# Optimization experiments

Measured on AMD Instinct MI355X. Metric: run time of the kernel, lower is better.

## Reference

```python
import jax, jax.numpy as jnp
import numpy as np

N_HEADS = 16
HEAD_DIM = 64  # dim=1024 / n_heads=16


def setup_inputs() -> dict:
    key = jax.random.key(0)
    ks = jax.random.split(key, 7)
    B, S, D = 4, 2048, 1024
    scale = 1.0 / np.sqrt(D)
    return {
        "q": jax.random.normal(ks[0], (B, S, D), jnp.float32),
        "k": jax.random.normal(ks[1], (B, S, D), jnp.float32),
        "v": jax.random.normal(ks[2], (B, S, D), jnp.float32),
        "Wq": jax.random.normal(ks[3], (D, D), jnp.float32) * scale,
        "Wk": jax.random.normal(ks[4], (D, D), jnp.float32) * scale,
        "Wv": jax.random.normal(ks[5], (D, D), jnp.float32) * scale,
        "Wo": jax.random.normal(ks[6], (D, D), jnp.float32) * scale,
    }


def reference(q, k, v, Wq, Wk, Wv, Wo):
    B, S, _ = q.shape
    H, Dh = N_HEADS, HEAD_DIM
    # linear projections (torch Linear: x @ W.T), reshape to [B, H, S, Dh]
    xq = (q @ Wq.T).reshape(B, S, H, Dh).transpose(0, 2, 1, 3)
    xk = (k @ Wk.T).reshape(B, S, H, Dh).transpose(0, 2, 1, 3)
    xv = (v @ Wv.T).reshape(B, S, H, Dh).transpose(0, 2, 1, 3)
    scores = jnp.einsum("bhsd,bhtd->bhst", xq, xk) / jnp.sqrt(jnp.float32(Dh))
    # causal mask: -inf above diagonal
    causal = jnp.triu(jnp.full((S, S), -jnp.inf, jnp.float32), k=1)
    scores = scores + causal[None, None]
    attn = jax.nn.softmax(scores.astype(jnp.float32), axis=-1).astype(xq.dtype)
    out = jnp.einsum("bhst,bhtd->bhsd", attn, xv)
    out = out.transpose(0, 2, 1, 3).reshape(B, S, H * Dh)
    return out @ Wo.T
```

## Files before the change

kernel.cpp:

```cpp
#include <hip/hip_runtime.h>
#include <hip/hip_bf16.h>

#define DI __device__ __forceinline__

typedef __attribute__((ext_vector_type(8))) short short8;
typedef __attribute__((ext_vector_type(4))) short short4v;
typedef __attribute__((ext_vector_type(4))) float f32x4;

#define QSCALE 0.180336885f

DI short f2bf(float f) {
  unsigned u = __builtin_bit_cast(unsigned, f);
  unsigned r = u + 0x7fffu + ((u >> 16) & 1u);
  return (short)(r >> 16);
}

DI float fexp2(float x) {
#if __has_builtin(__builtin_amdgcn_exp2f)
  return __builtin_amdgcn_exp2f(x);
#else
  return exp2f(x);
#endif
}

DI void gl16(const short* g, short* l) {
  __builtin_amdgcn_global_load_lds(
      (const __attribute__((address_space(1))) void*)g,
      (__attribute__((address_space(3))) void*)l, 16, 0, 0);
}

__global__ __launch_bounds__(256) void convert_w(
    const float* __restrict__ wq, const float* __restrict__ wk,
    const float* __restrict__ wv, const float* __restrict__ wo,
    short* __restrict__ dst) {
  int z = blockIdx.z;
  const float* src = (z == 0) ? wq : (z == 1) ? wk : (z == 2) ? wv : wo;
  short* d = dst + (size_t)z * 1024 * 1024;
  int i = (blockIdx.x * 256 + threadIdx.x) * 4;
  float4 f = *(const float4*)(src + i);
  short4v v;
  v[0] = f2bf(f.x); v[1] = f2bf(f.y); v[2] = f2bf(f.z); v[3] = f2bf(f.w);
  *(short4v*)(d + i) = v;
}

__global__ __launch_bounds__(256) void convert_x(
    const float* __restrict__ q, const float* __restrict__ k,
    const float* __restrict__ v, short* __restrict__ qb,
    short* __restrict__ kb, short* __restrict__ vb) {
  int z = blockIdx.z;
  const float* src = (z == 0) ? q : (z == 1) ? k : v;
  short* dst = (z == 0) ? qb : (z == 1) ? kb : vb;
  size_t i = ((size_t)blockIdx.x * 256 + threadIdx.x) * 8;
  float4 f0 = *(const float4*)(src + i);
  float4 f1 = *(const float4*)(src + i + 4);
  short8 o;
  o[0] = f2bf(f0.x); o[1] = f2bf(f0.y); o[2] = f2bf(f0.z); o[3] = f2bf(f0.w);
  o[4] = f2bf(f1.x); o[5] = f2bf(f1.y); o[6] = f2bf(f1.z); o[7] = f2bf(f1.w);
  *(short8*)(dst + i) = o;
}

__global__ __launch_bounds__(256) void convert_one(
    const float* __restrict__ src, short* __restrict__ dst) {
  size_t i = ((size_t)blockIdx.x * 256 + threadIdx.x) * 8;
  float4 f0 = *(const float4*)(src + i);
  float4 f1 = *(const float4*)(src + i + 4);
  short8 o;
  o[0] = f2bf(f0.x); o[1] = f2bf(f0.y); o[2] = f2bf(f0.z); o[3] = f2bf(f0.w);
  o[4] = f2bf(f1.x); o[5] = f2bf(f1.y); o[6] = f2bf(f1.z); o[7] = f2bf(f1.w);
  *(short8*)(dst + i) = o;
}

enum { OUT_F32 = 0, OUT_HEAD = 1, OUT_HEADT = 2 };

template <int OMODE>
DI void gemm_core(const short* __restrict__ A, const short* __restrict__ B,
                  void* __restrict__ Cp, float scale, int bm, int bn) {
  __shared__ __align__(16) short sA[128 * 64];
  __shared__ __align__(16) short sB[128 * 64];

  const int tid = threadIdx.x;
  const int lane = tid & 63;
  const int wid = tid >> 6;
  const int wm = wid >> 1, wn = wid & 1;
  const int l15 = lane & 15, lq = lane >> 4;
  const int lrr = lane >> 3;
  const int lch = lane & 7;

  f32x4 acc[4][4] = {};

  for (int k0 = 0; k0 < 1024; k0 += 64) {
#pragma unroll
    for (int i = 0; i < 4; ++i) {
      int r0 = wid * 32 + i * 8;
      int rr = r0 + lrr;
      int sc = (lch ^ (rr & 7)) << 3;
      gl16(A + (size_t)(bm + rr) * 1024 + k0 + sc, sA + r0 * 64);
      gl16(B + (size_t)(bn + rr) * 1024 + k0 + sc, sB + r0 * 64);
    }
    __syncthreads();

#pragma unroll
    for (int ks = 0; ks < 2; ++ks) {
      short8 a[4], b[4];
#pragma unroll
      for (int mt = 0; mt < 4; ++mt) {
        int row = wm * 64 + mt * 16 + l15;
        int off = (row * 128 + ks * 64 + lq * 16) ^ ((row & 7) << 4);
        a[mt] = *(const short8*)((const char*)sA + off);
      }
#pragma unroll
      for (int nt = 0; nt < 4; ++nt) {
        int row = wn * 64 + nt * 16 + l15;
        int off = (row * 128 + ks * 64 + lq * 16) ^ ((row & 7) << 4);
        b[nt] = *(const short8*)((const char*)sB + off);
      }
#pragma unroll
      for (int mt = 0; mt < 4; ++mt)
#pragma unroll
        for (int nt = 0; nt < 4; ++nt) {
          if (OMODE == OUT_HEADT)
            acc[mt][nt] = __builtin_amdgcn_mfma_f32_16x16x32_bf16(
                b[nt], a[mt], acc[mt][nt], 0, 0, 0);
          else
            acc[mt][nt] = __builtin_amdgcn_mfma_f32_16x16x32_bf16(
                a[mt], b[nt], acc[mt][nt], 0, 0, 0);
        }
    }
    __syncthreads();
  }

#pragma unroll
  for (int mt = 0; mt < 4; ++mt) {
#pragma unroll
    for (int nt = 0; nt < 4; ++nt) {
#pragma unroll
      for (int r = 0; r < 4; ++r) {
        float val = acc[mt][nt][r] * scale;
        if (OMODE == OUT_HEADT) {
          int f = bn + wn * 64 + nt * 16 + lq * 4 + r;
          int t = bm + wm * 64 + mt * 16 + l15;
          int bb = t >> 11, s = t & 2047;
          int h = f >> 6, dh = f & 63;
          ((short*)Cp)[((size_t)((bb * 16 + h) * 64 + dh)) * 2048 + s] = f2bf(val);
        } else {
          int rowg = bm + wm * 64 + mt * 16 + lq * 4 + r;
          int colg = bn + wn * 64 + nt * 16 + l15;
          if (OMODE == OUT_HEAD) {
            int bb = rowg >> 11, s = rowg & 2047;
            int h = colg >> 6, dh = colg & 63;
            ((short*)Cp)[((size_t)(bb * 16 + h) * 2048 + s) * 64 + dh] = f2bf(val);
          } else {
            ((float*)Cp)[(size_t)rowg * 1024 + colg] = val;
          }
        }
      }
    }
  }
}

DI void xcd_map(int id, int& bm, int& bn) {
  int xcd = id & 7, slot = id >> 3;
  int panel = xcd + 8 * (slot >> 3);
  int ntile = slot & 7;
  bm = panel * 128;
  bn = ntile * 128;
}

__global__ __launch_bounds__(256) void proj_gemm3(
    const short* __restrict__ qb, const short* __restrict__ kb,
    const short* __restrict__ vb, const short* __restrict__ wq,
    const short* __restrict__ wk, const short* __restrict__ wv,
    short* __restrict__ xq, short* __restrict__ xk, short* __restrict__ xvT) {
  int z = blockIdx.z;
  int bm, bn;
  xcd_map(blockIdx.x, bm, bn);
  if (z == 0) {
    gemm_core<OUT_HEAD>(qb, wq, xq, QSCALE, bm, bn);
  } else if (z == 1) {
    gemm_core<OUT_HEAD>(kb, wk, xk, 1.0f, bm, bn);
  } else {
    gemm_core<OUT_HEADT>(vb, wv, xvT, 1.0f, bm, bn);
  }
}

__global__ __launch_bounds__(256) void proj_oneN(
    const short* __restrict__ A, const short* __restrict__ B,
    short* __restrict__ C, float scale) {
  int bm, bn;
  xcd_map(blockIdx.x, bm, bn);
  gemm_core<OUT_HEAD>(A, B, C, scale, bm, bn);
}

__global__ __launch_bounds__(256) void proj_oneT(
    const short* __restrict__ A, const short* __restrict__ B,
    short* __restrict__ C, float scale) {
  int bm, bn;
  xcd_map(blockIdx.x, bm, bn);
  gemm_core<OUT_HEADT>(A, B, C, scale, bm, bn);
}

__global__ __launch_bounds__(256) void final_gemm(
    const short* __restrict__ oa, const short* __restrict__ wo,
    float* __restrict__ out) {
  int bm, bn;
  xcd_map(blockIdx.x, bm, bn);
  gemm_core<OUT_F32>(oa, wo, out, 1.0f, bm, bn);
}

__global__ __launch_bounds__(256, 4) void attn_k(
    const short* __restrict__ Xq, const short* __restrict__ Xk,
    const short* __restrict__ XvT, short* __restrict__ Oa) {
  __shared__ __align__(16) short sK[2][64 * 64];
  __shared__ __align__(16) short sVT[2][64 * 64];
  __shared__ __align__(16) short sP[4][16 * 64];

  const int tid = threadIdx.x;
  const int lane = tid & 63;
  const int wid = tid >> 6;
  const int l15 = lane & 15, lq = lane >> 4;
  const int bid = blockIdx.x;
  const int ipair = bid >> 6;
  const int bh = bid & 63;
  const int b = bh >> 4, h = bh & 15;

  const short* Q = Xq + (size_t)bh * 2048 * 64;
  const short* K = Xk + (size_t)bh * 2048 * 64;
  const short* VT = XvT + (size_t)bh * 64 * 2048;

  const int srow = tid >> 3;
  const int scol = (tid & 7) * 8;
  const int soff0 = (srow * 128 + scol * 2) ^ ((srow & 7) << 4);
  const int soff1 = ((srow + 32) * 128 + scol * 2) ^ ((srow & 7) << 4);

  short8 kreg[2], vreg[2];
  kreg[0] = *(const short8*)(K + (size_t)srow * 64 + scol);
  kreg[1] = *(const short8*)(K + (size_t)(srow + 32) * 64 + scol);
  vreg[0] = *(const short8*)(VT + (size_t)srow * 2048 + scol);
  vreg[1] = *(const short8*)(VT + (size_t)(srow + 32) * 2048 + scol);

  *(short8*)((char*)sK[0] + soff0) = kreg[0];
  *(short8*)((char*)sK[0] + soff1) = kreg[1];
  *(short8*)((char*)sVT[0] + soff0) = vreg[0];
  *(short8*)((char*)sVT[0] + soff1) = vreg[1];

  short* sPw = sP[wid];
  int p = 0;

  for (int seg = 0; seg < 2; ++seg) {
    const int qt = seg ? ipair : (31 - ipair);
    const int qrow0 = qt * 64 + wid * 16;
    const int qg = qrow0 + l15;

    short8 qf[2];
#pragma unroll
    for (int ks = 0; ks < 2; ++ks)
      qf[ks] = *(const short8*)(Q + (size_t)qg * 64 + ks * 32 + lq * 8);

    float m_run = -1e30f, l_run = 0.f;
    f32x4 acc[4] = {};

    for (int kt = 0; kt <= qt; ++kt) {
      const int kv0 = kt * 64;
      __syncthreads();

      int nkt = kt + 1, nseg = seg;
      if (nkt > qt) { nseg = seg + 1; nkt = 0; }
      const bool hn = (nseg < 2);
      if (hn) {
        const int kn = nkt * 64;
        kreg[0] = *(const short8*)(K + (size_t)(kn + srow) * 64 + scol);
        kreg[1] = *(const short8*)(K + (size_t)(kn + srow + 32) * 64 + scol);
        vreg[0] = *(const short8*)(VT + (size_t)srow * 2048 + kn + scol);
        vreg[1] = *(const short8*)(VT + (size_t)(srow + 32) * 2048 + kn + scol);
      }

      const char* bufK = (const char*)sK[p];
      const char* bufV = (const char*)sVT[p];

      f32x4 sc[4] = {};
      __builtin_amdgcn_s_setprio(1);
#pragma unroll
      for (int ks = 0; ks < 2; ++ks) {
        short8 kf[4];
#pragma unroll
        for (int nt = 0; nt < 4; ++nt) {
          int row = nt * 16 + l15;
          int off = (row * 128 + ks * 64 + lq * 16) ^ ((row & 7) << 4);
          kf[nt] = *(const short8*)(bufK + off);
        }
#pragma unroll
        for (int nt = 0; nt < 4; ++nt)
          sc[nt] = __builtin_amdgcn_mfma_f32_16x16x32_bf16(kf[nt], qf[ks], sc[nt], 0, 0, 0);
      }
      __builtin_amdgcn_s_setprio(0);

      float pv[4][4];
      float m = -1e30f;
      const bool diag = (kt == qt);
#pragma unroll
      for (int nt = 0; nt < 4; ++nt) {
#pragma unroll
        for (int r = 0; r < 4; ++r) {
          float s = sc[nt][r];
          if (diag && (kv0 + nt * 16 + lq * 4 + r > qg)) s = -1e30f;
          pv[nt][r] = s;
          m = fmaxf(m, s);
        }
      }
      m = fmaxf(m, __shfl_xor(m, 16));
      m = fmaxf(m, __shfl_xor(m, 32));

      if (!__all(m - m_run <= 8.0f)) {
        const float m_new = fmaxf(m_run, m);
        const float corr = fexp2(m_run - m_new);
        l_run *= corr;
#pragma unroll
        for (int mt = 0; mt < 4; ++mt)
#pragma unroll
          for (int r = 0; r < 4; ++r) acc[mt][r] *= corr;
        m_run = m_new;
      }

      float rsum = 0.f;
#pragma unroll
      for (int nt = 0; nt < 4; ++nt)
#pragma unroll
        for (int r = 0; r < 4; ++r) {
          float e = fexp2(pv[nt][r] - m_run);
          pv[nt][r] = e;
          rsum += e;
        }
      rsum += __shfl_xor(rsum, 16);
      rsum += __shfl_xor(rsum, 32);
      l_run += rsum;

#pragma unroll
      for (int nt = 0; nt < 4; ++nt) {
        short4v pw;
#pragma unroll
        for (int r = 0; r < 4; ++r) pw[r] = f2bf(pv[nt][r]);
        int off = (l15 * 128 + nt * 32 + lq * 8) ^ ((l15 & 7) << 4);
        *(short4v*)((char*)sPw + off) = pw;
      }

      __builtin_amdgcn_s_setprio(1);
#pragma unroll
      for (int ks = 0; ks < 2; ++ks) {
        int poff = (l15 * 128 + ks * 64 + lq * 16) ^ ((l15 & 7) << 4);
        short8 pf = *(const short8*)((const char*)sPw + poff);
#pragma unroll
        for (int mt = 0; mt < 4; ++mt) {
          int row = mt * 16 + l15;
          int voff = (row * 128 + ks * 64 + lq * 16) ^ ((row & 7) << 4);
          short8 vf = *(const short8*)(bufV + voff);
          acc[mt] = __builtin_amdgcn_mfma_f32_16x16x32_bf16(vf, pf, acc[mt], 0, 0, 0);
        }
      }
      __builtin_amdgcn_s_setprio(0);

      if (hn) {
        *(short8*)((char*)sK[p ^ 1] + soff0) = kreg[0];
        *(short8*)((char*)sK[p ^ 1] + soff1) = kreg[1];
        *(short8*)((char*)sVT[p ^ 1] + soff0) = vreg[0];
        *(short8*)((char*)sVT[p ^ 1] + soff1) = vreg[1];
      }
      p ^= 1;
    }

    const float rl = 1.0f / l_run;
    short* orow = Oa + ((size_t)(b * 2048 + qg)) * 1024 + h * 64;
#pragma unroll
    for (int mt = 0; mt < 4; ++mt) {
      short4v o;
#pragma unroll
      for (int r = 0; r < 4; ++r) o[r] = f2bf(acc[mt][r] * rl);
      *(short4v*)(orow + mt * 16 + lq * 4) = o;
    }
  }
}

extern "C" void kernel_launch(void* const* d_in, const int* in_sizes, int n_in,
                              void* d_out, int out_size, void* d_ws,
                              size_t ws_size, hipStream_t stream) {
  const float* q = (const float*)d_in[0];
  const float* k = (const float*)d_in[1];
  const float* v = (const float*)d_in[2];
  const float* Wq = (const float*)d_in[3];
  const float* Wk = (const float*)d_in[4];
  const float* Wv = (const float*)d_in[5];
  const float* Wo = (const float*)d_in[6];

  char* ws = (char*)d_ws;
  short* wq_b = (short*)(ws + (0ull << 20));
  short* wk_b = (short*)(ws + (2ull << 20));
  short* wv_b = (short*)(ws + (4ull << 20));
  short* wo_b = (short*)(ws + (6ull << 20));
  short* xq  = (short*)(ws + (8ull << 20));
  short* xk  = (short*)(ws + (24ull << 20));
  short* xvT = (short*)(ws + (56ull << 20));

  convert_w<<<dim3(1024, 1, 4), 256, 0, stream>>>(Wq, Wk, Wv, Wo, wq_b);

  if (ws_size >= (122ull << 20)) {
    short* qb = (short*)(ws + (72ull << 20));
    short* kb = (short*)(ws + (88ull << 20));
    short* vb = (short*)(ws + (104ull << 20));
    short* oa = qb;

    convert_x<<<dim3(4096, 1, 3), 256, 0, stream>>>(q, k, v, qb, kb, vb);
    proj_gemm3<<<dim3(512, 1, 3), 256, 0, stream>>>(qb, kb, vb, wq_b, wk_b,
                                                    wv_b, xq, xk, xvT);
    attn_k<<<dim3(1024), 256, 0, stream>>>(xq, xk, xvT, oa);
    final_gemm<<<dim3(512), 256, 0, stream>>>(oa, wo_b, (float*)d_out);
  } else {
    short* X = (short*)(ws + (8ull << 20));
    short* xq2 = (short*)(ws + (24ull << 20));
    short* xk2 = (short*)(ws + (40ull << 20));
    short* xvT2 = (short*)(ws + (56ull << 20));
    short* oa2 = (short*)(ws + (72ull << 20));

    convert_one<<<dim3(4096), 256, 0, stream>>>(q, X);
    proj_oneN<<<dim3(512), 256, 0, stream>>>(X, wq_b, xq2, QSCALE);
    convert_one<<<dim3(4096), 256, 0, stream>>>(k, X);
    proj_oneN<<<dim3(512), 256, 0, stream>>>(X, wk_b, xk2, 1.0f);
    convert_one<<<dim3(4096), 256, 0, stream>>>(v, X);
    proj_oneT<<<dim3(512), 256, 0, stream>>>(X, wv_b, xvT2, 1.0f);
    attn_k<<<dim3(1024), 256, 0, stream>>>(xq2, xk2, xvT2, oa2);
    final_gemm<<<dim3(512), 256, 0, stream>>>(oa2, wo_b, (float*)d_out);
  }
}
```

Before: 184.6 us.

## Use 128-row query tiles with 512-thread attention blocks sharing K/V tiles

The attention kernel now processes 128 query rows per block with 8 waves (512 threads) instead of 64 rows with 4 waves. Each staged K/V tile is therefore reused by twice as many queries, and the grid is halved. Waves whose rows lie entirely above a KV tile skip its compute, and masking is applied only on tiles that cross the diagonal. The bf16 conversion helper is switched to the library intrinsic. In exchange there are fewer blocks, load imbalance inside a block along the diagonal, and register pressure under launch bounds of 512 threads with 4 blocks per CU.

```diff
diff --git a/kernel.cpp b/kernel.cpp
--- a/kernel.cpp
+++ b/kernel.cpp
@@ -10,9 +10,8 @@
 #define QSCALE 0.180336885f
 
 DI short f2bf(float f) {
-  unsigned u = __builtin_bit_cast(unsigned, f);
-  unsigned r = u + 0x7fffu + ((u >> 16) & 1u);
-  return (short)(r >> 16);
+  __hip_bfloat16 h = __float2bfloat16(f);
+  return __builtin_bit_cast(short, h);
 }
 
 DI float fexp2(float x) {
@@ -207,12 +206,12 @@
   gemm_core<OUT_F32>(oa, wo, out, 1.0f, bm, bn);
 }
 
-__global__ __launch_bounds__(256, 4) void attn_k(
+__global__ __launch_bounds__(512, 4) void attn_k(
     const short* __restrict__ Xq, const short* __restrict__ Xk,
     const short* __restrict__ XvT, short* __restrict__ Oa) {
   __shared__ __align__(16) short sK[2][64 * 64];
   __shared__ __align__(16) short sVT[2][64 * 64];
-  __shared__ __align__(16) short sP[4][16 * 64];
+  __shared__ __align__(16) short sP[8][16 * 64];
 
   const int tid = threadIdx.x;
   const int lane = tid & 63;
@@ -229,27 +228,24 @@
 
   const int srow = tid >> 3;
   const int scol = (tid & 7) * 8;
-  const int soff0 = (srow * 128 + scol * 2) ^ ((srow & 7) << 4);
-  const int soff1 = ((srow + 32) * 128 + scol * 2) ^ ((srow & 7) << 4);
-
-  short8 kreg[2], vreg[2];
-  kreg[0] = *(const short8*)(K + (size_t)srow * 64 + scol);
-  kreg[1] = *(const short8*)(K + (size_t)(srow + 32) * 64 + scol);
-  vreg[0] = *(const short8*)(VT + (size_t)srow * 2048 + scol);
-  vreg[1] = *(const short8*)(VT + (size_t)(srow + 32) * 2048 + scol);
-
-  *(short8*)((char*)sK[0] + soff0) = kreg[0];
-  *(short8*)((char*)sK[0] + soff1) = kreg[1];
-  *(short8*)((char*)sVT[0] + soff0) = vreg[0];
-  *(short8*)((char*)sVT[0] + soff1) = vreg[1];
+  const int soff = (srow * 128 + scol * 2) ^ ((srow & 7) << 4);
+
+  short8 kreg, vreg;
+  kreg = *(const short8*)(K + (size_t)srow * 64 + scol);
+  vreg = *(const short8*)(VT + (size_t)srow * 2048 + scol);
+
+  *(short8*)((char*)sK[0] + soff) = kreg;
+  *(short8*)((char*)sVT[0] + soff) = vreg;
 
   short* sPw = sP[wid];
   int p = 0;
 
   for (int seg = 0; seg < 2; ++seg) {
-    const int qt = seg ? ipair : (31 - ipair);
-    const int qrow0 = qt * 64 + wid * 16;
-    const int qg = qrow0 + l15;
+    const int qt = seg ? ipair : (15 - ipair);
+    const int qfirst = qt * 128 + wid * 16;
+    const int qg = qfirst + l15;
+    const int qlast = qfirst + 15;
+    const int ntile = 2 * qt + 2;
 
     short8 qf[2];
 #pragma unroll
@@ -259,110 +255,121 @@
     float m_run = -1e30f, l_run = 0.f;
     f32x4 acc[4] = {};
 
-    for (int kt = 0; kt <= qt; ++kt) {
+    for (int kt = 0; kt < ntile; ++kt) {
       const int kv0 = kt * 64;
       __syncthreads();
 
       int nkt = kt + 1, nseg = seg;
-      if (nkt > qt) { nseg = seg + 1; nkt = 0; }
+      if (nkt >= ntile) { nseg = seg + 1; nkt = 0; }
       const bool hn = (nseg < 2);
       if (hn) {
         const int kn = nkt * 64;
-        kreg[0] = *(const short8*)(K + (size_t)(kn + srow) * 64 + scol);
-        kreg[1] = *(const short8*)(K + (size_t)(kn + srow + 32) * 64 + scol);
-        vreg[0] = *(const short8*)(VT + (size_t)srow * 2048 + kn + scol);
-        vreg[1] = *(const short8*)(VT + (size_t)(srow + 32) * 2048 + kn + scol);
-      }
-
-      const char* bufK = (const char*)sK[p];
-      const char* bufV = (const char*)sVT[p];
-
-      f32x4 sc[4] = {};
-      __builtin_amdgcn_s_setprio(1);
-#pragma unroll
-      for (int ks = 0; ks < 2; ++ks) {
-        short8 kf[4];
+        kreg = *(const short8*)(K + (size_t)(kn + srow) * 64 + scol);
+        vreg = *(const short8*)(VT + (size_t)srow * 2048 + kn + scol);
+      }
+
+      const bool fullmask = (kv0 > qlast);
+      if (!fullmask) {
+        const bool needmask = (kv0 + 63 > qfirst);
+        const char* bufK = (const char*)sK[p];
+        const char* bufV = (const char*)sVT[p];
+
+        f32x4 sc[4] = {};
+        __builtin_amdgcn_s_setprio(1);
+#pragma unroll
+        for (int ks = 0; ks < 2; ++ks) {
+          short8 kf[4];
+#pragma unroll
+          for (int nt = 0; nt < 4; ++nt) {
+            int row = nt * 16 + l15;
+            int off = (row * 128 + ks * 64 + lq * 16) ^ ((row & 7) << 4);
+            kf[nt] = *(const short8*)(bufK + off);
+          }
+#pragma unroll
+          for (int nt = 0; nt < 4; ++nt)
+            sc[nt] = __builtin_amdgcn_mfma_f32_16x16x32_bf16(kf[nt], qf[ks],
+                                                             sc[nt], 0, 0, 0);
+        }
+        __builtin_amdgcn_s_setprio(0);
+
+        float pv[4][4];
+        float m = -1e30f;
+        if (needmask) {
+#pragma unroll
+          for (int nt = 0; nt < 4; ++nt)
+#pragma unroll
+            for (int r = 0; r < 4; ++r) {
+              float s = sc[nt][r];
+              if (kv0 + nt * 16 + lq * 4 + r > qg) s = -1e30f;
+              pv[nt][r] = s;
+              m = fmaxf(m, s);
+            }
+        } else {
+#pragma unroll
+          for (int nt = 0; nt < 4; ++nt)
+#pragma unroll
+            for (int r = 0; r < 4; ++r) {
+              float s = sc[nt][r];
+              pv[nt][r] = s;
+              m = fmaxf(m, s);
+            }
+        }
+        m = fmaxf(m, __shfl_xor(m, 16));
+        m = fmaxf(m, __shfl_xor(m, 32));
+
+        if (!__all(m - m_run <= 8.0f)) {
+          const float m_new = fmaxf(m_run, m);
+          const float corr = fexp2(m_run - m_new);
+          l_run *= corr;
+#pragma unroll
+          for (int mt = 0; mt < 4; ++mt)
+#pragma unroll
+            for (int r = 0; r < 4; ++r) acc[mt][r] *= corr;
+          m_run = m_new;
+        }
+
+        float rsum = 0.f;
+#pragma unroll
+        for (int nt = 0; nt < 4; ++nt)
+#pragma unroll
+          for (int r = 0; r < 4; ++r) {
+            float e = fexp2(pv[nt][r] - m_run);
+            pv[nt][r] = e;
+            rsum += e;
+          }
+        rsum += __shfl_xor(rsum, 16);
+        rsum += __shfl_xor(rsum, 32);
+        l_run += rsum;
+
 #pragma unroll
         for (int nt = 0; nt < 4; ++nt) {
-          int row = nt * 16 + l15;
-          int off = (row * 128 + ks * 64 + lq * 16) ^ ((row & 7) << 4);
-          kf[nt] = *(const short8*)(bufK + off);
-        }
-#pragma unroll
-        for (int nt = 0; nt < 4; ++nt)
-          sc[nt] = __builtin_amdgcn_mfma_f32_16x16x32_bf16(kf[nt], qf[ks], sc[nt], 0, 0, 0);
-      }
-      __builtin_amdgcn_s_setprio(0);
-
-      float pv[4][4];
-      float m = -1e30f;
-      const bool diag = (kt == qt);
-#pragma unroll
-      for (int nt = 0; nt < 4; ++nt) {
-#pragma unroll
-        for (int r = 0; r < 4; ++r) {
-          float s = sc[nt][r];
-          if (diag && (kv0 + nt * 16 + lq * 4 + r > qg)) s = -1e30f;
-          pv[nt][r] = s;
-          m = fmaxf(m, s);
-        }
-      }
-      m = fmaxf(m, __shfl_xor(m, 16));
-      m = fmaxf(m, __shfl_xor(m, 32));
-
-      if (!__all(m - m_run <= 8.0f)) {
-        const float m_new = fmaxf(m_run, m);
-        const float corr = fexp2(m_run - m_new);
-        l_run *= corr;
-#pragma unroll
-        for (int mt = 0; mt < 4; ++mt)
-#pragma unroll
-          for (int r = 0; r < 4; ++r) acc[mt][r] *= corr;
-        m_run = m_new;
-      }
-
-      float rsum = 0.f;
-#pragma unroll
-      for (int nt = 0; nt < 4; ++nt)
-#pragma unroll
-        for (int r = 0; r < 4; ++r) {
-          float e = fexp2(pv[nt][r] - m_run);
-          pv[nt][r] = e;
-          rsum += e;
-        }
-      rsum += __shfl_xor(rsum, 16);
-      rsum += __shfl_xor(rsum, 32);
-      l_run += rsum;
-
-#pragma unroll
-      for (int nt = 0; nt < 4; ++nt) {
-        short4v pw;
-#pragma unroll
-        for (int r = 0; r < 4; ++r) pw[r] = f2bf(pv[nt][r]);
-        int off = (l15 * 128 + nt * 32 + lq * 8) ^ ((l15 & 7) << 4);
-        *(short4v*)((char*)sPw + off) = pw;
-      }
-
-      __builtin_amdgcn_s_setprio(1);
-#pragma unroll
-      for (int ks = 0; ks < 2; ++ks) {
-        int poff = (l15 * 128 + ks * 64 + lq * 16) ^ ((l15 & 7) << 4);
-        short8 pf = *(const short8*)((const char*)sPw + poff);
-#pragma unroll
-        for (int mt = 0; mt < 4; ++mt) {
-          int row = mt * 16 + l15;
-          int voff = (row * 128 + ks * 64 + lq * 16) ^ ((row & 7) << 4);
-          short8 vf = *(const short8*)(bufV + voff);
-          acc[mt] = __builtin_amdgcn_mfma_f32_16x16x32_bf16(vf, pf, acc[mt], 0, 0, 0);
-        }
-      }
-      __builtin_amdgcn_s_setprio(0);
+          short4v pw;
+#pragma unroll
+          for (int r = 0; r < 4; ++r) pw[r] = f2bf(pv[nt][r]);
+          int off = (l15 * 128 + nt * 32 + lq * 8) ^ ((l15 & 7) << 4);
+          *(short4v*)((char*)sPw + off) = pw;
+        }
+
+        __builtin_amdgcn_s_setprio(1);
+#pragma unroll
+        for (int ks = 0; ks < 2; ++ks) {
+          int poff = (l15 * 128 + ks * 64 + lq * 16) ^ ((l15 & 7) << 4);
+          short8 pf = *(const short8*)((const char*)sPw + poff);
+#pragma unroll
+          for (int mt = 0; mt < 4; ++mt) {
+            int row = mt * 16 + l15;
+            int voff = (row * 128 + ks * 64 + lq * 16) ^ ((row & 7) << 4);
+            short8 vf = *(const short8*)(bufV + voff);
+            acc[mt] = __builtin_amdgcn_mfma_f32_16x16x32_bf16(vf, pf, acc[mt],
+                                                              0, 0, 0);
+          }
+        }
+        __builtin_amdgcn_s_setprio(0);
+      }
 
       if (hn) {
-        *(short8*)((char*)sK[p ^ 1] + soff0) = kreg[0];
-        *(short8*)((char*)sK[p ^ 1] + soff1) = kreg[1];
-        *(short8*)((char*)sVT[p ^ 1] + soff0) = vreg[0];
-        *(short8*)((char*)sVT[p ^ 1] + soff1) = vreg[1];
+        *(short8*)((char*)sK[p ^ 1] + soff) = kreg;
+        *(short8*)((char*)sVT[p ^ 1] + soff) = vreg;
       }
       p ^= 1;
     }
@@ -410,7 +417,7 @@
     convert_x<<<dim3(4096, 1, 3), 256, 0, stream>>>(q, k, v, qb, kb, vb);
     proj_gemm3<<<dim3(512, 1, 3), 256, 0, stream>>>(qb, kb, vb, wq_b, wk_b,
                                                     wv_b, xq, xk, xvT);
-    attn_k<<<dim3(1024), 256, 0, stream>>>(xq, xk, xvT, oa);
+    attn_k<<<dim3(512), 512, 0, stream>>>(xq, xk, xvT, oa);
     final_gemm<<<dim3(512), 256, 0, stream>>>(oa, wo_b, (float*)d_out);
   } else {
     short* X = (short*)(ws + (8ull << 20));
@@ -425,7 +432,7 @@
     proj_oneN<<<dim3(512), 256, 0, stream>>>(X, wk_b, xk2, 1.0f);
     convert_one<<<dim3(4096), 256, 0, stream>>>(v, X);
     proj_oneT<<<dim3(512), 256, 0, stream>>>(X, wv_b, xvT2, 1.0f);
-    attn_k<<<dim3(1024), 256, 0, stream>>>(xq2, xk2, xvT2, oa2);
+    attn_k<<<dim3(512), 512, 0, stream>>>(xq2, xk2, xvT2, oa2);
     final_gemm<<<dim3(512), 256, 0, stream>>>(oa2, wo_b, (float*)d_out);
   }
 }
```

After: 178.2 us. 1.04x faster.
